# Kernel optimization log

Measured on AMD Instinct MI355X. Metric: run time of the kernel, lower is better.

Reference implementation:

```python
import jax, jax.numpy as jnp
import numpy as np

H, D = 8, 64
LN_EPS = 1e-5

def elu_p1(x):
    return jax.nn.elu(x) + 1.0

def sum_norm(x):
    return x / jnp.sum(x, axis=-1, keepdims=True)

def setup_inputs() -> dict:
    key = jax.random.key(0)
    k1, k2, k3 = jax.random.split(key, 3)
    slen, bsz, in_dim = 1024, 32, 512
    x = jax.random.normal(k1, (slen, bsz, in_dim), dtype=jnp.float32)
    ln_gamma = jnp.ones((in_dim,), dtype=jnp.float32)
    ln_beta = jnp.zeros((in_dim,), dtype=jnp.float32)
    # Linear weights stored as [in, out] (transposed vs torch) and fan-in scaled
    w_slow = jax.random.normal(k2, (in_dim, H * (3 * D + 1)), dtype=jnp.float32) / np.sqrt(in_dim)
    w_out = jax.random.normal(k3, (H * D, in_dim), dtype=jnp.float32) / np.sqrt(H * D)
    return {"x": x, "ln_gamma": ln_gamma, "ln_beta": ln_beta, "w_slow": w_slow, "w_out": w_out}

def reference(x, ln_gamma, ln_beta, w_slow, w_out):
    slen, bsz, in_dim = x.shape
    # LayerNorm
    mu = jnp.mean(x, axis=-1, keepdims=True)
    var = jnp.mean((x - mu) ** 2, axis=-1, keepdims=True)
    h = (x - mu) * jax.lax.rsqrt(var + LN_EPS) * ln_gamma + ln_beta
    # slow net projection -> q, k, v, beta per head
    qkvb = (h @ w_slow).reshape(slen, bsz, H, 3 * D + 1)
    q, k, v, beta = jnp.split(qkvb, [D, 2 * D, 3 * D], axis=-1)
    beta = jax.nn.sigmoid(beta)            # [slen, bsz, H, 1]
    q = sum_norm(elu_p1(q))                # [slen, bsz, H, D]
    k = sum_norm(elu_p1(k))
    # delta-rule fast-weight recurrence over time
    W0 = jnp.zeros((bsz, H, D, D), dtype=x.dtype)
    def step(W, inp):
        q_t, k_t, v_t, b_t = inp           # [bsz,H,D], [bsz,H,D], [bsz,H,D], [bsz,H,1]
        v_old = jnp.einsum('bhij,bhj->bhi', W, k_t)
        upd = b_t * (v_t - v_old)          # [bsz,H,D]
        W = W + upd[..., :, None] * k_t[..., None, :]
        o_t = jnp.einsum('bhij,bhj->bhi', W, q_t)
        return W, o_t
    _, outs = jax.lax.scan(step, W0, (q, k, v, beta))  # outs [slen, bsz, H, D]
    out = outs.reshape(slen, bsz, H * D) @ w_out       # [slen, bsz, in_dim]
    return x + out
```

## Files before the change

### kernel.cpp

```cpp
#include <hip/hip_runtime.h>
#include <cstdint>

using short8  = __attribute__((ext_vector_type(8))) short;
using ushort8 = __attribute__((ext_vector_type(8))) unsigned short;
using short4v = __attribute__((ext_vector_type(4))) short;
using f32x4   = __attribute__((ext_vector_type(4))) float;

#define H_    8
#define SLEN  1024
#define BSZ   32
#define INDIM 512
#define NQKV  1544
#define NPAD2 1792
#define MROWS 32768
#define PB    72

#define GLOAD16(gp, lp) __builtin_amdgcn_global_load_lds( \
    (const __attribute__((address_space(1))) void*)(gp),  \
    (__attribute__((address_space(3))) void*)(lp), 16, 0, 0)

#define VMCNT8() do { asm volatile("s_waitcnt vmcnt(8)" ::: "memory"); \
                      __builtin_amdgcn_sched_barrier(0); } while (0)
#define VMCNT0() do { asm volatile("s_waitcnt vmcnt(0)" ::: "memory"); \
                      __builtin_amdgcn_sched_barrier(0); } while (0)
#define SBAR()   do { __builtin_amdgcn_sched_barrier(0); \
                      __builtin_amdgcn_s_barrier(); \
                      __builtin_amdgcn_sched_barrier(0); } while (0)

static __device__ __forceinline__ float bf2f(unsigned short s) {
    return __uint_as_float(((unsigned int)s) << 16);
}
#if defined(__BF16_MANT_DIG__)
static __device__ __forceinline__ unsigned short f2bf(float f) {
    union { __bf16 b; unsigned short u; } cv;
    cv.b = (__bf16)f;
    return cv.u;
}
#else
static __device__ __forceinline__ unsigned short f2bf(float f) {
    unsigned int u = __float_as_uint(f);
    u += 0x7FFFu + ((u >> 16) & 1u);
    return (unsigned short)(u >> 16);
}
#endif

__global__ __launch_bounds__(256) void ln_kernel(const float* __restrict__ x,
                                                 const float* __restrict__ gamma,
                                                 const float* __restrict__ betap,
                                                 unsigned short* __restrict__ h) {
    int row = blockIdx.x * 4 + (threadIdx.x >> 6);
    int l   = threadIdx.x & 63;
    const f32x4* xr = (const f32x4*)(x + (size_t)row * INDIM);
    f32x4 a = xr[l * 2], b = xr[l * 2 + 1];
    float s = 0.f, sq = 0.f;
    #pragma unroll
    for (int j = 0; j < 4; ++j) { s += a[j]; sq += a[j] * a[j]; }
    #pragma unroll
    for (int j = 0; j < 4; ++j) { s += b[j]; sq += b[j] * b[j]; }
    #pragma unroll
    for (int off = 32; off; off >>= 1) { s += __shfl_xor(s, off); sq += __shfl_xor(sq, off); }
    float mean = s * (1.f / 512.f);
    float var  = sq * (1.f / 512.f) - mean * mean;
    float rstd = rsqrtf(var + 1e-5f);
    const f32x4* g4 = (const f32x4*)gamma;
    const f32x4* b4 = (const f32x4*)betap;
    f32x4 g0 = g4[l * 2], g1 = g4[l * 2 + 1], e0 = b4[l * 2], e1 = b4[l * 2 + 1];
    short8 o;
    #pragma unroll
    for (int j = 0; j < 4; ++j) o[j]     = (short)f2bf((a[j] - mean) * rstd * g0[j] + e0[j]);
    #pragma unroll
    for (int j = 0; j < 4; ++j) o[4 + j] = (short)f2bf((b[j] - mean) * rstd * g1[j] + e1[j]);
    ((short8*)(h + (size_t)row * INDIM))[l] = o;
}

__global__ __launch_bounds__(256) void cvt_wslow(const float* __restrict__ w,
                                                 unsigned short* __restrict__ wT) {
    int idx = blockIdx.x * 256 + threadIdx.x;
    int n = idx >> 9, k = idx & 511;
    int c;
    if (n < 512)       c = (n >> 6) * 193 + (n & 63);
    else if (n < 1024) c = ((n - 512) >> 6) * 193 + 64 + (n & 63);
    else if (n < 1536) c = ((n - 1024) >> 6) * 193 + 128 + (n & 63);
    else if (n < 1544) c = (n - 1536) * 193 + 192;
    else               c = -1;
    wT[idx] = (c >= 0) ? f2bf(w[(size_t)k * NQKV + c]) : (unsigned short)0;
}
__global__ __launch_bounds__(256) void cvt_wout(const float* __restrict__ w,
                                                unsigned short* __restrict__ wT) {
    int idx = blockIdx.x * 256 + threadIdx.x;
    int n = idx >> 9, k = idx & 511;
    wT[idx] = f2bf(w[(size_t)k * 512 + n]);
}

__global__ __launch_bounds__(512, 2) void gemm_qkv(const unsigned short* __restrict__ A,
                                                   const unsigned short* __restrict__ BT,
                                                   unsigned short* __restrict__ qn,
                                                   unsigned short* __restrict__ kn,
                                                   unsigned short* __restrict__ vn,
                                                   float* __restrict__ bet) {
    __shared__ unsigned short As[2][256 * 64];
    __shared__ unsigned short Bs[2][256 * 64];
    const int tid = threadIdx.x;
    const int id = blockIdx.y * 7 + blockIdx.x;
    const int newid = (id & 7) * 112 + (id >> 3);
    const int bx = newid % 7;
    const int n0 = bx * 256;
    const int m0 = (newid / 7) * 256;
    const int w = tid >> 6, l = tid & 63;
    const int wm = w >> 2, wn = w & 3;
    const int lr = l & 15, lk8 = (l >> 4) * 8;
    f32x4 acc[8][4] = {};

    auto STAGE = [&](int buf, int kt) {
        #pragma unroll
        for (int c2 = 0; c2 < 4; ++c2) {
            int idx = c2 * 512 + tid;
            int row = idx >> 3, kc2 = (idx & 7) * 8;
            int lb = (c2 * 512 + (tid & 448)) * 8;
            GLOAD16(A  + (size_t)(m0 + row) * INDIM + kt + kc2, &As[buf][lb]);
            GLOAD16(BT + (size_t)(n0 + row) * INDIM + kt + kc2, &Bs[buf][lb]);
        }
    };
    auto COMPUTE = [&](int buf) {
        short8 bf2[4][2];
        #pragma unroll
        for (int ni = 0; ni < 4; ++ni)
            #pragma unroll
            for (int kk = 0; kk < 2; ++kk)
                bf2[ni][kk] = *(const short8*)&Bs[buf][(wn * 64 + ni * 16 + lr) * 64 + kk * 32 + lk8];
        #pragma unroll
        for (int p = 0; p < 4; ++p) {
            short8 af[2][2];
            #pragma unroll
            for (int d = 0; d < 2; ++d)
                #pragma unroll
                for (int kk = 0; kk < 2; ++kk)
                    af[d][kk] = *(const short8*)&As[buf][(wm * 128 + (2 * p + d) * 16 + lr) * 64 + kk * 32 + lk8];
            #pragma unroll
            for (int d = 0; d < 2; ++d)
                #pragma unroll
                for (int ni = 0; ni < 4; ++ni)
                    #pragma unroll
                    for (int kk = 0; kk < 2; ++kk)
                        acc[2 * p + d][ni] =
                            __builtin_amdgcn_mfma_f32_16x16x32_bf16(af[d][kk], bf2[ni][kk], acc[2 * p + d][ni], 0, 0, 0);
        }
    };

    STAGE(0, 0);
    STAGE(1, 64);
    #pragma unroll
    for (int tp = 0; tp < 4; ++tp) {
        VMCNT8();
        SBAR();
        COMPUTE(0);
        SBAR();
        if (tp < 3) {
            STAGE(0, (2 * tp + 2) * 64);
            VMCNT8();
        } else {
            VMCNT0();
        }
        SBAR();
        COMPUTE(1);
        SBAR();
        if (tp < 3) STAGE(1, (2 * tp + 3) * 64);
    }

    const int g = l >> 4, cc = l & 15;
    const int colbase = n0 + wn * 64;
    if (bx < 6) {
        const int reg  = colbase >> 9;
        const int head = (colbase >> 6) & 7;
        unsigned short* dst = (reg == 0) ? qn : (reg == 1) ? kn : vn;
        #pragma unroll
        for (int mi = 0; mi < 8; ++mi) {
            #pragma unroll
            for (int j = 0; j < 4; ++j) {
                int row = m0 + wm * 128 + mi * 16 + g * 4 + j;
                int s = row >> 5, b = row & 31;
                size_t base = ((size_t)(b * H_ + head) * SLEN + s) * 64;
                float e0 = acc[mi][0][j], e1 = acc[mi][1][j], e2 = acc[mi][2][j], e3 = acc[mi][3][j];
                if (reg < 2) {
                    e0 = e0 > 0.f ? e0 + 1.f : __expf(e0);
                    e1 = e1 > 0.f ? e1 + 1.f : __expf(e1);
                    e2 = e2 > 0.f ? e2 + 1.f : __expf(e2);
                    e3 = e3 > 0.f ? e3 + 1.f : __expf(e3);
                    float ssum = (e0 + e1) + (e2 + e3);
                    ssum += __shfl_xor(ssum, 1);
                    ssum += __shfl_xor(ssum, 2);
                    ssum += __shfl_xor(ssum, 4);
                    ssum += __shfl_xor(ssum, 8);
                    float inv = 1.f / ssum;
                    e0 *= inv; e1 *= inv; e2 *= inv; e3 *= inv;
                }
                dst[base +  0 + cc] = f2bf(e0);
                dst[base + 16 + cc] = f2bf(e1);
                dst[base + 32 + cc] = f2bf(e2);
                dst[base + 48 + cc] = f2bf(e3);
            }
        }
    } else {
        if (wn == 0 && cc < 8) {
            #pragma unroll
            for (int mi = 0; mi < 8; ++mi)
                #pragma unroll
                for (int j = 0; j < 4; ++j) {
                    int row = m0 + wm * 128 + mi * 16 + g * 4 + j;
                    int s = row >> 5, b = row & 31;
                    float v = acc[mi][0][j];
                    bet[(size_t)(b * H_ + cc) * SLEN + s] = 1.f / (1.f + __expf(-v));
                }
        }
    }
}

__global__ __launch_bounds__(512, 2) void gemm_out(const unsigned short* __restrict__ A,
                                                   const unsigned short* __restrict__ BT,
                                                   const float* __restrict__ X,
                                                   float* __restrict__ outf) {
    __shared__ unsigned short As[2][256 * 64];
    __shared__ unsigned short Bs[2][256 * 64];
    const int tid = threadIdx.x;
    const int id = blockIdx.y * 2 + blockIdx.x;
    const int newid = (id & 7) * 32 + (id >> 3);
    const int n0 = (newid & 1) * 256;
    const int m0 = (newid >> 1) * 256;
    const int w = tid >> 6, l = tid & 63;
    const int wm = w >> 2, wn = w & 3;
    const int lr = l & 15, lk8 = (l >> 4) * 8;
    f32x4 acc[8][4] = {};

    auto STAGE = [&](int buf, int kt) {
        #pragma unroll
        for (int c2 = 0; c2 < 4; ++c2) {
            int idx = c2 * 512 + tid;
            int row = idx >> 3, kc2 = (idx & 7) * 8;
            int lb = (c2 * 512 + (tid & 448)) * 8;
            GLOAD16(A  + (size_t)(m0 + row) * INDIM + kt + kc2, &As[buf][lb]);
            GLOAD16(BT + (size_t)(n0 + row) * INDIM + kt + kc2, &Bs[buf][lb]);
        }
    };
    auto COMPUTE = [&](int buf) {
        short8 bf2[4][2];
        #pragma unroll
        for (int ni = 0; ni < 4; ++ni)
            #pragma unroll
            for (int kk = 0; kk < 2; ++kk)
                bf2[ni][kk] = *(const short8*)&Bs[buf][(wn * 64 + ni * 16 + lr) * 64 + kk * 32 + lk8];
        #pragma unroll
        for (int p = 0; p < 4; ++p) {
            short8 af[2][2];
            #pragma unroll
            for (int d = 0; d < 2; ++d)
                #pragma unroll
                for (int kk = 0; kk < 2; ++kk)
                    af[d][kk] = *(const short8*)&As[buf][(wm * 128 + (2 * p + d) * 16 + lr) * 64 + kk * 32 + lk8];
            #pragma unroll
            for (int d = 0; d < 2; ++d)
                #pragma unroll
                for (int ni = 0; ni < 4; ++ni)
                    #pragma unroll
                    for (int kk = 0; kk < 2; ++kk)
                        acc[2 * p + d][ni] =
                            __builtin_amdgcn_mfma_f32_16x16x32_bf16(af[d][kk], bf2[ni][kk], acc[2 * p + d][ni], 0, 0, 0);
        }
    };

    STAGE(0, 0);
    STAGE(1, 64);
    #pragma unroll
    for (int tp = 0; tp < 4; ++tp) {
        VMCNT8();
        SBAR();
        COMPUTE(0);
        SBAR();
        if (tp < 3) {
            STAGE(0, (2 * tp + 2) * 64);
            VMCNT8();
        } else {
            VMCNT0();
        }
        SBAR();
        COMPUTE(1);
        SBAR();
        if (tp < 3) STAGE(1, (2 * tp + 3) * 64);
    }

    const int g = l >> 4, cc = l & 15;
    #pragma unroll
    for (int mi = 0; mi < 8; ++mi)
        #pragma unroll
        for (int ni = 0; ni < 4; ++ni)
            #pragma unroll
            for (int j = 0; j < 4; ++j) {
                int row = m0 + wm * 128 + mi * 16 + g * 4 + j;
                int col = n0 + wn * 64 + ni * 16 + cc;
                size_t o = (size_t)row * 512 + col;
                outf[o] = X[o] + acc[mi][ni][j];
            }
}

__global__ __launch_bounds__(512, 4) void fwtiles(const unsigned short* __restrict__ qn,
                                                  const unsigned short* __restrict__ kn,
                                                  const unsigned short* __restrict__ vn,
                                                  const float* __restrict__ beta,
                                                  unsigned short* __restrict__ tiles,
                                                  unsigned short* __restrict__ outs) {
    __shared__ unsigned short Ax[64 * PB], Atr[64 * PB], Pw[64 * PB], Pwtr[64 * PB];
    __shared__ unsigned short Z0[128 * PB], Z1[128 * PB];
    __shared__ float bv[64];
    const int bx = blockIdx.x;
    const int bh = bx >> 4, c = bx & 15;
    const int b = bh >> 3, h = bh & 7;
    const int c0 = c * 64;
    const int tid = threadIdx.x;
    const int w = tid >> 6, l = tid & 63;
    const int mw = w & 3, nh = w >> 2;
    const int lr = l & 15, lk = (l >> 4) << 3, rb = (l >> 4) << 2;
    const unsigned short* kc = kn + ((size_t)bh * SLEN + c0) * 64;
    const unsigned short* qc = qn + ((size_t)bh * SLEN + c0) * 64;
    const unsigned short* vc = vn + ((size_t)bh * SLEN + c0) * 64;
    const float* bb = beta + (size_t)bh * SLEN + c0;

    {
        #pragma unroll
        for (int i = 0; i < 2; ++i) {
            int idx = i * 512 + tid;
            int row = idx >> 3, seg = idx & 7;
            const unsigned short* src = (row < 64) ? (vc + (size_t)row * 64 + seg * 8)
                                                   : (kc + (size_t)(row - 64) * 64 + seg * 8);
            *(ushort8*)&Z1[row * PB + seg * 8] = *(const ushort8*)src;
        }
        if (tid < 64) bv[tid] = bb[tid];
        ushort8 z8 = {};
        for (int i = tid; i < 576; i += 512) { ((ushort8*)Ax)[i] = z8; ((ushort8*)Atr)[i] = z8; }
    }
    __syncthreads();

    auto ldb = [&](const unsigned short* M, int m, int kk) -> short8 {
        return *(const short8*)&M[(m * 16 + lr) * PB + kk * 32 + lk];
    };

    {
        const int zoff2 = (w >> 2) * 64;
        const int tbase = (w & 3) * 16;
        const float sgn = (w >= 4) ? -1.f : 1.f;
        ushort8 b0v, b1v;
        #pragma unroll
        for (int i = 0; i < 16; ++i) {
            int r = w * 16 + i;
            float val = sgn * bv[tbase + i] * bf2f(Z1[r * PB + l]);
            unsigned short uv = f2bf(val);
            if (i < 8) b0v[i] = uv; else b1v[i - 8] = uv;
        }
        *(ushort8*)&Z0[(zoff2 + l) * PB + tbase]     = b0v;
        *(ushort8*)&Z0[(zoff2 + l) * PB + tbase + 8] = b1v;
    }
    {
        const int pm[10] = {0, 1, 1, 2, 2, 2, 3, 3, 3, 3};
        const int pn[10] = {0, 0, 1, 0, 1, 2, 0, 1, 2, 3};
        for (int pi = w; pi < 10; pi += 8) {
            int m = pm[pi], n = pn[pi];
            short8 ka0 = *(const short8*)&Z1[(64 + 16 * m + lr) * PB + lk];
            short8 ka1 = *(const short8*)&Z1[(64 + 16 * m + lr) * PB + 32 + lk];
            short8 kb0 = *(const short8*)&Z1[(64 + 16 * n + lr) * PB + lk];
            short8 kb1 = *(const short8*)&Z1[(64 + 16 * n + lr) * PB + 32 + lk];
            f32x4 a = {};
            a = __builtin_amdgcn_mfma_f32_16x16x32_bf16(ka0, kb0, a, 0, 0, 0);
            a = __builtin_amdgcn_mfma_f32_16x16x32_bf16(ka1, kb1, a, 0, 0, 0);
            f32x4 btm = *(const f32x4*)&bv[16 * m + rb];
            short4v pk;
            #pragma unroll
            for (int j = 0; j < 4; ++j) {
                int tt = 16 * m + rb + j, s = 16 * n + lr;
                unsigned short v = (s < tt) ? f2bf(-btm[j] * a[j]) : (unsigned short)0;
                Ax[tt * PB + s] = v;
                pk[j] = (short)v;
            }
            *(short4v*)&Atr[(16 * n + lr) * PB + 16 * m + rb] = pk;
        }
    }
    __syncthreads();

    auto zprod = [&](const unsigned short* Xb, int p, const unsigned short* Zs, unsigned short* Zd) {
        const bool msk0 = (16 * mw + 15 >= p), msk1 = (16 * mw + 15 - 32 >= p);
        short8 xf0, xf1;
        if (msk0) xf0 = ldb(Xb, mw, 0);
        if (msk1) xf1 = ldb(Xb, mw, 1);
        #pragma unroll
        for (int ni = 0; ni < 4; ++ni) {
            int n = nh * 4 + ni;
            short4v zi = *(const short4v*)&Zs[(16 * n + lr) * PB + 16 * mw + rb];
            f32x4 a;
            #pragma unroll
            for (int j = 0; j < 4; ++j) a[j] = bf2f((unsigned short)zi[j]);
            if (msk0) a = __builtin_amdgcn_mfma_f32_16x16x32_bf16(xf0, ldb(Zs, n, 0), a, 0, 0, 0);
            if (msk1) a = __builtin_amdgcn_mfma_f32_16x16x32_bf16(xf1, ldb(Zs, n, 1), a, 0, 0, 0);
            short4v zo;
            #pragma unroll
            for (int j = 0; j < 4; ++j) zo[j] = (short)f2bf(a[j]);
            *(short4v*)&Zd[(16 * n + lr) * PB + 16 * mw + rb] = zo;
        }
    };
    auto powp = [&](const unsigned short* Ps, const unsigned short* Pstr, int p,
                    unsigned short* Pd, unsigned short* Pdtr, bool wrTr) {
        const bool x0 = (16 * mw + 15 >= p), x1 = (16 * mw + 15 - 32 >= p);
        short8 xf0, xf1;
        if (x0) xf0 = ldb(Ps, mw, 0);
        if (x1) xf1 = ldb(Ps, mw, 1);
        #pragma unroll
        for (int ni = 0; ni < 2; ++ni) {
            int n = nh * 2 + ni;
            const bool y0 = (31 - 16 * n >= p), y1 = (63 - 16 * n >= p);
            f32x4 a = {};
            if (x0 && y0) a = __builtin_amdgcn_mfma_f32_16x16x32_bf16(xf0, ldb(Pstr, n, 0), a, 0, 0, 0);
            if (x1 && y1) a = __builtin_amdgcn_mfma_f32_16x16x32_bf16(xf1, ldb(Pstr, n, 1), a, 0, 0, 0);
            short4v pk;
            #pragma unroll
            for (int j = 0; j < 4; ++j) {
                unsigned short v = f2bf(a[j]);
                Pd[(16 * mw + rb + j) * PB + 16 * n + lr] = v;
                pk[j] = (short)v;
            }
            if (wrTr) *(short4v*)&Pdtr[(16 * n + lr) * PB + 16 * mw + rb] = pk;
        }
    };

    zprod(Ax, 1, Z0, Z1);  powp(Ax, Atr, 1, Pw, Pwtr, true);   __syncthreads();
    zprod(Pw, 2, Z1, Z0);  powp(Pw, Pwtr, 2, Ax, Atr, true);   __syncthreads();
    zprod(Ax, 4, Z0, Z1);  powp(Ax, Atr, 4, Pw, Pwtr, true);   __syncthreads();
    zprod(Pw, 8, Z1, Z0);  powp(Pw, Pwtr, 8, Ax, Atr, true);   __syncthreads();
    zprod(Ax, 16, Z0, Z1); powp(Ax, Atr, 16, Pw, Pwtr, false); __syncthreads();
    zprod(Pw, 32, Z1, Z0);
    __syncthreads();

    {
        #pragma unroll
        for (int i = 0; i < 2; ++i) {
            int idx = i * 512 + tid;
            int row = idx >> 3, seg = idx & 7;
            const unsigned short* src = (row < 64) ? (qc + (size_t)row * 64 + seg * 8)
                                                   : (kc + (size_t)(row - 64) * 64 + seg * 8);
            *(ushort8*)&Z1[row * PB + seg * 8] = *(const ushort8*)src;
        }
    }
    __syncthreads();

    {
        short8 qa0 = *(const short8*)&Z1[(16 * mw + lr) * PB + lk];
        short8 qa1 = *(const short8*)&Z1[(16 * mw + lr) * PB + 32 + lk];
        #pragma unroll
        for (int ni = 0; ni < 2; ++ni) {
            int n = nh * 2 + ni;
            short8 kb0 = *(const short8*)&Z1[(64 + 16 * n + lr) * PB + lk];
            short8 kb1 = *(const short8*)&Z1[(64 + 16 * n + lr) * PB + 32 + lk];
            f32x4 a = {};
            a = __builtin_amdgcn_mfma_f32_16x16x32_bf16(qa0, kb0, a, 0, 0, 0);
            a = __builtin_amdgcn_mfma_f32_16x16x32_bf16(qa1, kb1, a, 0, 0, 0);
            #pragma unroll
            for (int j = 0; j < 4; ++j) {
                int tt = 16 * mw + rb + j, s = 16 * n + lr;
                Ax[tt * PB + s] = (s <= tt) ? f2bf(a[j]) : (unsigned short)0;
            }
        }
        ushort8 kv;
        #pragma unroll
        for (int j = 0; j < 8; ++j)
            kv[j] = Z1[(64 + w * 8 + j) * PB + l];
        *(ushort8*)&Pwtr[l * PB + w * 8] = kv;
    }
    __syncthreads();

    {
        unsigned short* tb = tiles + ((size_t)bh * 16 + c) * 12288;
        short8 pA0 = ldb(Ax, mw, 0), pA1 = ldb(Ax, mw, 1);
        short8 zA0 = ldb(Z0, mw, 0), zA1 = ldb(Z0, mw, 1);
        short8 kt0 = ldb(Pwtr, mw, 0), kt1 = ldb(Pwtr, mw, 1);
        #pragma unroll
        for (int ni = 0; ni < 2; ++ni) {
            int n = nh * 2 + ni;
            f32x4 aN = {};
            aN = __builtin_amdgcn_mfma_f32_16x16x32_bf16(zA0, ldb(Pwtr, n, 0), aN, 0, 0, 0);
            aN = __builtin_amdgcn_mfma_f32_16x16x32_bf16(zA1, ldb(Pwtr, n, 1), aN, 0, 0, 0);
            f32x4 aM = {};
            aM = __builtin_amdgcn_mfma_f32_16x16x32_bf16(kt0, ldb(Z0, 4 + n, 0), aM, 0, 0, 0);
            aM = __builtin_amdgcn_mfma_f32_16x16x32_bf16(kt1, ldb(Z0, 4 + n, 1), aM, 0, 0, 0);
            f32x4 aG;
            #pragma unroll
            for (int j = 0; j < 4; ++j) aG[j] = bf2f(Z1[(16 * mw + rb + j) * PB + 16 * n + lr]);
            aG = __builtin_amdgcn_mfma_f32_16x16x32_bf16(pA0, ldb(Z0, 4 + n, 0), aG, 0, 0, 0);
            aG = __builtin_amdgcn_mfma_f32_16x16x32_bf16(pA1, ldb(Z0, 4 + n, 1), aG, 0, 0, 0);
            f32x4 aP = {};
            aP = __builtin_amdgcn_mfma_f32_16x16x32_bf16(pA0, ldb(Z0, n, 0), aP, 0, 0, 0);
            aP = __builtin_amdgcn_mfma_f32_16x16x32_bf16(pA1, ldb(Z0, n, 1), aP, 0, 0, 0);
            #pragma unroll
            for (int j = 0; j < 4; ++j) {
                int r = 16 * mw + rb + j, cl = 16 * n + lr;
                tb[r * 64 + cl]        = f2bf(aM[j]);
                tb[4096 + r * 64 + cl] = f2bf(aG[j]);
                tb[8192 + r * 64 + cl] = f2bf(aN[j]);
                outs[((size_t)(c0 + r) * BSZ + b) * 512 + h * 64 + cl] = f2bf(aP[j]);
            }
        }
    }
}

__global__ __launch_bounds__(256) void fwscan_w(const unsigned short* __restrict__ tiles,
                                                unsigned short* __restrict__ wchk) {
    __shared__ float Wf[64 * 68];
    const int bh = blockIdx.x;
    const int tid = threadIdx.x;
    const int w = tid >> 6, l = tid & 63;
    const int lr = l & 15, lk = (l >> 4) << 3, rb = (l >> 4) << 2;
    const int cr = l >> 3, cc8 = (l & 7) * 8;
    #pragma unroll
    for (int j = 0; j < 16; ++j) Wf[(16 * w + j) * 68 + l] = 0.f;

    const unsigned short* tb0 = tiles + (size_t)bh * 16 * 12288;
    unsigned short* wc0 = wchk + (size_t)bh * 16 * 4096;

    auto loadc = [&](short8 (&MT)[4][2], unsigned short (&NV)[4][4], int c) {
        const unsigned short* tb = tb0 + (size_t)c * 12288;
        #pragma unroll
        for (int n = 0; n < 4; ++n) {
            MT[n][0] = *(const short8*)(tb + (size_t)(16 * n + lr) * 64 + lk);
            MT[n][1] = *(const short8*)(tb + (size_t)(16 * n + lr) * 64 + 32 + lk);
            #pragma unroll
            for (int j = 0; j < 4; ++j)
                NV[n][j] = tb[8192 + (size_t)(16 * w + rb + j) * 64 + 16 * n + lr];
        }
    };
    auto stepc = [&](short8 (&MT)[4][2], unsigned short (&NV)[4][4], int c) {
        #pragma unroll
        for (int half = 0; half < 2; ++half) {
            int row = 16 * w + half * 8 + cr;
            const float* p = &Wf[row * 68 + cc8];
            f32x4 x0 = *(const f32x4*)p, x1 = *(const f32x4*)(p + 4);
            ushort8 o;
            #pragma unroll
            for (int j = 0; j < 4; ++j) { o[j] = f2bf(x0[j]); o[4 + j] = f2bf(x1[j]); }
            *(ushort8*)(wc0 + (size_t)c * 4096 + row * 64 + cc8) = o;
        }
        short8 wf0, wf1;
        {
            const float* p0 = &Wf[(16 * w + lr) * 68 + lk];
            f32x4 a0 = *(const f32x4*)p0, b0 = *(const f32x4*)(p0 + 4);
            f32x4 a1 = *(const f32x4*)(p0 + 32), b1 = *(const f32x4*)(p0 + 36);
            #pragma unroll
            for (int j = 0; j < 4; ++j) {
                wf0[j] = (short)f2bf(a0[j]); wf0[4 + j] = (short)f2bf(b0[j]);
                wf1[j] = (short)f2bf(a1[j]); wf1[4 + j] = (short)f2bf(b1[j]);
            }
        }
        #pragma unroll
        for (int n = 0; n < 4; ++n) {
            f32x4 a;
            #pragma unroll
            for (int j = 0; j < 4; ++j)
                a[j] = Wf[(16 * w + rb + j) * 68 + 16 * n + lr] + bf2f(NV[n][j]);
            a = __builtin_amdgcn_mfma_f32_16x16x32_bf16(wf0, MT[n][0], a, 0, 0, 0);
            a = __builtin_amdgcn_mfma_f32_16x16x32_bf16(wf1, MT[n][1], a, 0, 0, 0);
            #pragma unroll
            for (int j = 0; j < 4; ++j) Wf[(16 * w + rb + j) * 68 + 16 * n + lr] = a[j];
        }
    };

    short8 mtA[4][2], mtB[4][2];
    unsigned short nvA[4][4], nvB[4][4];
    loadc(mtA, nvA, 0);
    #pragma unroll 1
    for (int cc = 0; cc < 8; ++cc) {
        int c = 2 * cc;
        if (c + 1 < 16) loadc(mtB, nvB, c + 1);
        stepc(mtA, nvA, c);
        if (c + 2 < 16) loadc(mtA, nvA, c + 2);
        stepc(mtB, nvB, c + 1);
    }
}

__global__ __launch_bounds__(256) void fw_o(const unsigned short* __restrict__ tiles,
                                            const unsigned short* __restrict__ wchk,
                                            unsigned short* __restrict__ outs) {
    __shared__ unsigned short Ot[64 * 72];
    const int c = blockIdx.x + 1;
    const int bh = blockIdx.y;
    const int b = bh >> 3, h = bh & 7;
    const int c0 = c * 64;
    const int tid = threadIdx.x;
    const int w = tid >> 6, l = tid & 63;
    const int lr = l & 15, lk = (l >> 4) << 3, rb = (l >> 4) << 2;
    const unsigned short* G  = tiles + ((size_t)bh * 16 + c) * 12288 + 4096;
    const unsigned short* W0 = wchk + ((size_t)bh * 16 + c) * 4096;

    #pragma unroll
    for (int i = 0; i < 2; ++i) {
        int idx = i * 256 + tid;
        int t = idx >> 3, d0 = (idx & 7) * 8;
        *(ushort8*)&Ot[t * 72 + d0] =
            *(const ushort8*)(outs + ((size_t)(c0 + t) * BSZ + b) * 512 + h * 64 + d0);
    }
    __syncthreads();

    short8 g0 = *(const short8*)(G + (size_t)(16 * w + lr) * 64 + lk);
    short8 g1 = *(const short8*)(G + (size_t)(16 * w + lr) * 64 + 32 + lk);
    #pragma unroll
    for (int n = 0; n < 4; ++n) {
        short8 wf0 = *(const short8*)(W0 + (size_t)(16 * n + lr) * 64 + lk);
        short8 wf1 = *(const short8*)(W0 + (size_t)(16 * n + lr) * 64 + 32 + lk);
        f32x4 a;
        #pragma unroll
        for (int j = 0; j < 4; ++j) a[j] = bf2f(Ot[(16 * w + rb + j) * 72 + 16 * n + lr]);
        a = __builtin_amdgcn_mfma_f32_16x16x32_bf16(g0, wf0, a, 0, 0, 0);
        a = __builtin_amdgcn_mfma_f32_16x16x32_bf16(g1, wf1, a, 0, 0, 0);
        #pragma unroll
        for (int j = 0; j < 4; ++j) Ot[(16 * w + rb + j) * 72 + 16 * n + lr] = f2bf(a[j]);
    }
    __syncthreads();

    #pragma unroll
    for (int i = 0; i < 2; ++i) {
        int idx = i * 256 + tid;
        int t = idx >> 3, d0 = (idx & 7) * 8;
        *(ushort8*)(outs + ((size_t)(c0 + t) * BSZ + b) * 512 + h * 64 + d0) =
            *(const ushort8*)&Ot[t * 72 + d0];
    }
}

extern "C" void kernel_launch(void* const* d_in, const int* in_sizes, int n_in,
                              void* d_out, int out_size, void* d_ws, size_t ws_size,
                              hipStream_t stream) {
    const float* x      = (const float*)d_in[0];
    const float* g      = (const float*)d_in[1];
    const float* be     = (const float*)d_in[2];
    const float* w_slow = (const float*)d_in[3];
    const float* w_out  = (const float*)d_in[4];
    float* out = (float*)d_out;
    char* ws = (char*)d_ws;

    unsigned short* h    = (unsigned short*)(ws);
    unsigned short* outs = (unsigned short*)(ws);
    unsigned short* qn   = (unsigned short*)(ws + 33554432);
    unsigned short* wchk = (unsigned short*)(ws + 33554432);
    unsigned short* kn   = (unsigned short*)(ws + 67108864);
    unsigned short* vn   = (unsigned short*)(ws + 100663296);
    float*          bet  = (float*)         (ws + 134217728);
    unsigned short* wsT  = (unsigned short*)(ws + 135266304);
    unsigned short* woT  = (unsigned short*)(ws + 137101312);
    unsigned short* tiles= (unsigned short*)(ws + 137625600);

    if (ws_size < 238288896) return;

    ln_kernel<<<8192, 256, 0, stream>>>(x, g, be, h);
    cvt_wslow<<<(NPAD2 * 512) / 256, 256, 0, stream>>>(w_slow, wsT);
    cvt_wout<<<(512 * 512) / 256, 256, 0, stream>>>(w_out, woT);
    gemm_qkv<<<dim3(7, MROWS / 256), 512, 0, stream>>>(h, wsT, qn, kn, vn, bet);
    fwtiles<<<BSZ * H_ * 16, 512, 0, stream>>>(qn, kn, vn, bet, tiles, outs);
    fwscan_w<<<BSZ * H_, 256, 0, stream>>>(tiles, wchk);
    fw_o<<<dim3(15, BSZ * H_), 256, 0, stream>>>(tiles, wchk, outs);
    gemm_out<<<dim3(2, MROWS / 256), 512, 0, stream>>>(outs, woT, x, out);
}
```

Measured before the change: 337.5 us.

## Transpose weights through LDS tiles and stage QKV epilogue for coalesced stores

The weight conversion kernels now transpose through a padded 64x65 shared-memory tile, so both the fp32 reads and the bf16 writes are coalesced instead of strided. The QKV GEMM epilogue writes its activated bf16 outputs into the reused shared-memory buffer with an XOR swizzle, then issues 16-byte vector stores of whole rows into the head-major q/k/v layouts. The goal is to replace scattered 2-byte global stores with wide coalesced ones. The cost is an extra barrier and an LDS round trip at the end of the GEMM.

```diff
diff --git a/kernel.cpp b/kernel.cpp
--- a/kernel.cpp
+++ b/kernel.cpp
@@ -73,23 +73,59 @@
     ((short8*)(h + (size_t)row * INDIM))[l] = o;
 }
 
-__global__ __launch_bounds__(256) void cvt_wslow(const float* __restrict__ w,
-                                                 unsigned short* __restrict__ wT) {
-    int idx = blockIdx.x * 256 + threadIdx.x;
-    int n = idx >> 9, k = idx & 511;
-    int c;
-    if (n < 512)       c = (n >> 6) * 193 + (n & 63);
-    else if (n < 1024) c = ((n - 512) >> 6) * 193 + 64 + (n & 63);
-    else if (n < 1536) c = ((n - 1024) >> 6) * 193 + 128 + (n & 63);
-    else if (n < 1544) c = (n - 1536) * 193 + 192;
-    else               c = -1;
-    wT[idx] = (c >= 0) ? f2bf(w[(size_t)k * NQKV + c]) : (unsigned short)0;
+__global__ __launch_bounds__(256) void cvt_wslow2(const float* __restrict__ w,
+                                                  unsigned short* __restrict__ wT) {
+    __shared__ float T[64][65];
+    const int tid = threadIdx.x;
+    const int k0 = blockIdx.x * 64;
+    const int ng = blockIdx.y;
+    if (ng < 24) {
+        const int cbase = (ng & 7) * 193 + (ng >> 3) * 64;
+        const int nn = tid & 63, kk = tid >> 6;
+        #pragma unroll
+        for (int i = 0; i < 16; ++i)
+            T[kk + 4 * i][nn] = w[(size_t)(k0 + kk + 4 * i) * NQKV + cbase + nn];
+        __syncthreads();
+        const int kseg = (tid & 7) * 8;
+        #pragma unroll
+        for (int i = 0; i < 2; ++i) {
+            int nn2 = i * 32 + (tid >> 3);
+            ushort8 o;
+            #pragma unroll
+            for (int j = 0; j < 8; ++j) o[j] = f2bf(T[kseg + j][nn2]);
+            *(ushort8*)&wT[(size_t)(ng * 64 + nn2) * 512 + k0 + kseg] = o;
+        }
+    } else {
+        for (int i = 0; i < 64; ++i) {
+            int gid = i * 256 + tid;
+            int nn = gid >> 6, kk = gid & 63;
+            int n = 1536 + nn;
+            unsigned short v = 0;
+            if (n < 1544) v = f2bf(w[(size_t)(k0 + kk) * NQKV + (n - 1536) * 193 + 192]);
+            wT[(size_t)n * 512 + k0 + kk] = v;
+        }
+    }
 }
 __global__ __launch_bounds__(256) void cvt_wout(const float* __restrict__ w,
                                                 unsigned short* __restrict__ wT) {
-    int idx = blockIdx.x * 256 + threadIdx.x;
-    int n = idx >> 9, k = idx & 511;
-    wT[idx] = f2bf(w[(size_t)k * 512 + n]);
+    __shared__ float T[64][65];
+    const int tid = threadIdx.x;
+    const int k0 = blockIdx.x * 64;
+    const int n0 = blockIdx.y * 64;
+    const int nn = tid & 63, kk = tid >> 6;
+    #pragma unroll
+    for (int i = 0; i < 16; ++i)
+        T[kk + 4 * i][nn] = w[(size_t)(k0 + kk + 4 * i) * 512 + n0 + nn];
+    __syncthreads();
+    const int kseg = (tid & 7) * 8;
+    #pragma unroll
+    for (int i = 0; i < 2; ++i) {
+        int nn2 = i * 32 + (tid >> 3);
+        ushort8 o;
+        #pragma unroll
+        for (int j = 0; j < 8; ++j) o[j] = f2bf(T[kseg + j][nn2]);
+        *(ushort8*)&wT[(size_t)(n0 + nn2) * 512 + k0 + kseg] = o;
+    }
 }
 
 __global__ __launch_bounds__(512, 2) void gemm_qkv(const unsigned short* __restrict__ A,
@@ -98,8 +134,7 @@
                                                    unsigned short* __restrict__ kn,
                                                    unsigned short* __restrict__ vn,
                                                    float* __restrict__ bet) {
-    __shared__ unsigned short As[2][256 * 64];
-    __shared__ unsigned short Bs[2][256 * 64];
+    __shared__ unsigned short SMEM[65536];
     const int tid = threadIdx.x;
     const int id = blockIdx.y * 7 + blockIdx.x;
     const int newid = (id & 7) * 112 + (id >> 3);
@@ -117,17 +152,19 @@
             int idx = c2 * 512 + tid;
             int row = idx >> 3, kc2 = (idx & 7) * 8;
             int lb = (c2 * 512 + (tid & 448)) * 8;
-            GLOAD16(A  + (size_t)(m0 + row) * INDIM + kt + kc2, &As[buf][lb]);
-            GLOAD16(BT + (size_t)(n0 + row) * INDIM + kt + kc2, &Bs[buf][lb]);
+            GLOAD16(A  + (size_t)(m0 + row) * INDIM + kt + kc2, &SMEM[buf * 16384 + lb]);
+            GLOAD16(BT + (size_t)(n0 + row) * INDIM + kt + kc2, &SMEM[32768 + buf * 16384 + lb]);
         }
     };
     auto COMPUTE = [&](int buf) {
+        const unsigned short* As = &SMEM[buf * 16384];
+        const unsigned short* Bs = &SMEM[32768 + buf * 16384];
         short8 bf2[4][2];
         #pragma unroll
         for (int ni = 0; ni < 4; ++ni)
             #pragma unroll
             for (int kk = 0; kk < 2; ++kk)
-                bf2[ni][kk] = *(const short8*)&Bs[buf][(wn * 64 + ni * 16 + lr) * 64 + kk * 32 + lk8];
+                bf2[ni][kk] = *(const short8*)&Bs[(wn * 64 + ni * 16 + lr) * 64 + kk * 32 + lk8];
         #pragma unroll
         for (int p = 0; p < 4; ++p) {
             short8 af[2][2];
@@ -135,7 +172,7 @@
             for (int d = 0; d < 2; ++d)
                 #pragma unroll
                 for (int kk = 0; kk < 2; ++kk)
-                    af[d][kk] = *(const short8*)&As[buf][(wm * 128 + (2 * p + d) * 16 + lr) * 64 + kk * 32 + lk8];
+                    af[d][kk] = *(const short8*)&As[(wm * 128 + (2 * p + d) * 16 + lr) * 64 + kk * 32 + lk8];
             #pragma unroll
             for (int d = 0; d < 2; ++d)
                 #pragma unroll
@@ -170,16 +207,11 @@
     const int g = l >> 4, cc = l & 15;
     const int colbase = n0 + wn * 64;
     if (bx < 6) {
-        const int reg  = colbase >> 9;
-        const int head = (colbase >> 6) & 7;
-        unsigned short* dst = (reg == 0) ? qn : (reg == 1) ? kn : vn;
+        const int reg = colbase >> 9;
         #pragma unroll
         for (int mi = 0; mi < 8; ++mi) {
             #pragma unroll
             for (int j = 0; j < 4; ++j) {
-                int row = m0 + wm * 128 + mi * 16 + g * 4 + j;
-                int s = row >> 5, b = row & 31;
-                size_t base = ((size_t)(b * H_ + head) * SLEN + s) * 64;
                 float e0 = acc[mi][0][j], e1 = acc[mi][1][j], e2 = acc[mi][2][j], e3 = acc[mi][3][j];
                 if (reg < 2) {
                     e0 = e0 > 0.f ? e0 + 1.f : __expf(e0);
@@ -194,11 +226,28 @@
                     float inv = 1.f / ssum;
                     e0 *= inv; e1 *= inv; e2 *= inv; e3 *= inv;
                 }
-                dst[base +  0 + cc] = f2bf(e0);
-                dst[base + 16 + cc] = f2bf(e1);
-                dst[base + 32 + cc] = f2bf(e2);
-                dst[base + 48 + cc] = f2bf(e3);
+                int lrow = wm * 128 + mi * 16 + g * 4 + j;
+                int key = ((lrow >> 2) & 3) << 4;
+                int cb = wn * 64;
+                SMEM[lrow * 256 + ((cb +  0 + cc) ^ key)] = f2bf(e0);
+                SMEM[lrow * 256 + ((cb + 16 + cc) ^ key)] = f2bf(e1);
+                SMEM[lrow * 256 + ((cb + 32 + cc) ^ key)] = f2bf(e2);
+                SMEM[lrow * 256 + ((cb + 48 + cc) ^ key)] = f2bf(e3);
             }
+        }
+        SBAR();
+        unsigned short* dst = (reg == 0) ? qn : (reg == 1) ? kn : vn;
+        #pragma unroll
+        for (int it = 0; it < 16; ++it) {
+            int idx = it * 512 + tid;
+            int lrow = idx >> 5, seg = idx & 31;
+            int key = ((lrow >> 2) & 3) << 4;
+            ushort8 v = *(const ushort8*)&SMEM[lrow * 256 + ((seg * 8) ^ key)];
+            int grow = m0 + lrow;
+            int s = grow >> 5, b = grow & 31;
+            int gcol = n0 + seg * 8;
+            int hd = (gcol >> 6) & 7, d0 = gcol & 63;
+            *(ushort8*)(dst + ((size_t)(b * H_ + hd) * SLEN + s) * 64 + d0) = v;
         }
     } else {
         if (wn == 0 && cc < 8) {
@@ -652,8 +701,8 @@
     if (ws_size < 238288896) return;
 
     ln_kernel<<<8192, 256, 0, stream>>>(x, g, be, h);
-    cvt_wslow<<<(NPAD2 * 512) / 256, 256, 0, stream>>>(w_slow, wsT);
-    cvt_wout<<<(512 * 512) / 256, 256, 0, stream>>>(w_out, woT);
+    cvt_wslow2<<<dim3(8, 25), 256, 0, stream>>>(w_slow, wsT);
+    cvt_wout<<<dim3(8, 8), 256, 0, stream>>>(w_out, woT);
     gemm_qkv<<<dim3(7, MROWS / 256), 512, 0, stream>>>(h, wsT, qn, kn, vn, bet);
     fwtiles<<<BSZ * H_ * 16, 512, 0, stream>>>(qn, kn, vn, bet, tiles, outs);
     fwscan_w<<<BSZ * H_, 256, 0, stream>>>(tiles, wchk);
```

Result: no change. 339.8 us (+0.7%).
